# Optimization experiments

Measured on AMD Instinct MI355X. Metric: run time of the kernel, lower is better.

Reference implementation:

```python
import jax, jax.numpy as jnp
import numpy as np

PATCH = 14
NPS = 26  # num_patches_per_side = 364 // 14


def setup_inputs() -> dict:
    key = jax.random.key(0)
    k0, k1, k2 = jax.random.split(key, 3)
    B, C, H, W, D = 32, 3, 364, 364, 1152
    pixel_values = jax.random.normal(k0, (B, C, H, W), dtype=jnp.float32)
    # variable-resolution rectangle masks (top-left aligned, NaViT style)
    rng = np.random.default_rng(0)
    nbh = rng.integers(NPS // 2, NPS + 1, size=B)
    nbw = rng.integers(NPS // 2, NPS + 1, size=B)
    mask = np.zeros((B, NPS, NPS), dtype=bool)
    for i in range(B):  # setup-time only, not part of reference compute
        mask[i, : nbh[i], : nbw[i]] = True
    patch_attention_mask = jnp.asarray(mask)
    conv_w = jax.random.normal(k1, (D, C, PATCH, PATCH), dtype=jnp.float32) * 0.02
    conv_b = jnp.zeros((D,), dtype=jnp.float32)
    pos_emb = jax.random.normal(k2, (NPS * NPS, D), dtype=jnp.float32) * 0.02
    return {
        "pixel_values": pixel_values,
        "patch_attention_mask": patch_attention_mask,
        "conv_w": conv_w,
        "conv_b": conv_b,
        "pos_emb": pos_emb,
    }


def _position_ids(mask):
    # mask: [B, Hp, Wp] bool, True on a top-left rectangle per sample
    B, Hp, Wp = mask.shape
    boundaries = jnp.arange(1, NPS, dtype=jnp.float32) / NPS  # NPS-1 edges
    nb_h = mask[:, :, 0].sum(axis=1)  # [B]
    nb_w = mask[:, 0, :].sum(axis=1)  # [B]
    eps = 1.0 - 1e-6
    frac_h = jnp.arange(Hp, dtype=jnp.float32)[None, :] / nb_h[:, None].astype(jnp.float32) * eps
    frac_w = jnp.arange(Wp, dtype=jnp.float32)[None, :] / nb_w[:, None].astype(jnp.float32) * eps
    # torch.bucketize(right=True) == searchsorted side='right'
    bh = jnp.searchsorted(boundaries, frac_h, side="right")  # [B, Hp]
    bw = jnp.searchsorted(boundaries, frac_w, side="right")  # [B, Wp]
    pos = bh[:, :, None] * NPS + bw[:, None, :]  # [B, Hp, Wp]
    pos = pos.reshape(B, Hp * Wp)
    return jnp.where(mask.reshape(B, -1), pos, 0)


def reference(pixel_values, patch_attention_mask, conv_w, conv_b, pos_emb):
    # patch embedding: conv2d stride=patch, padding VALID
    patch_embeds = jax.lax.conv_general_dilated(
        pixel_values, conv_w,
        window_strides=(PATCH, PATCH), padding="VALID",
        dimension_numbers=("NCHW", "OIHW", "NCHW"),
    ) + conv_b[None, :, None, None]  # [B, D, Hp, Wp]
    B, D, Hp, Wp = patch_embeds.shape
    embeddings = patch_embeds.reshape(B, D, Hp * Wp).transpose(0, 2, 1)  # [B, P, D]
    position_ids = _position_ids(patch_attention_mask)  # [B, P]
    return embeddings + pos_emb[position_ids]
```

## Files before the change

kernel.cpp:

```cpp
#include <hip/hip_runtime.h>
#include <stdint.h>

typedef __attribute__((ext_vector_type(8))) short short8;
typedef __attribute__((ext_vector_type(4))) float f32x4;

#define B_      32
#define C_      3
#define HW_     364
#define D_      1152
#define NPS_    26
#define P_      676
#define K_      588
#define KP_     608
#define KC_     19
#define MT_     64
#define NT_     384
#define AS_     616
#define NP_     21632
#define MBLK_   338
#define NBLK_   3
#define NT16_   72

static __device__ __forceinline__ unsigned short f2bf(float x) {
  unsigned u = __float_as_uint(x);
  u += 0x7fffu + ((u >> 16) & 1u);
  return (unsigned short)(u >> 16);
}

__global__ void prep_weights(const float* __restrict__ w,
                             unsigned short* __restrict__ whi) {
  int idx = blockIdx.x * 256 + threadIdx.x;
  if (idx >= NT16_ * KC_ * 64 * 8) return;
  int e    = idx & 7;
  int lane = (idx >> 3) & 63;
  int t    = idx >> 9;
  int kc   = t % KC_;
  int nt   = t / KC_;
  int n = nt * 16 + (lane & 15);
  int k = kc * 32 + (lane >> 4) * 8 + e;
  float x = (k < K_) ? w[n * K_ + k] : 0.0f;
  whi[idx] = f2bf(x);
}

__global__ void prep_pos(const void* __restrict__ maskp, int* __restrict__ pos_ids) {
  const int word0 = ((const int*)maskp)[0];
  int mode;
  if (word0 == 1) mode = 0;
  else if (word0 == 0x3F800000) mode = 2;
  else mode = 1;

  int idx = blockIdx.x * 256 + threadIdx.x;
  if (idx >= NP_) return;
  const int b = idx / P_;
  const int p = idx - b * P_;
  const int base = b * P_;

  auto get = [&](int i) -> int {
    if (mode == 0) return ((const int*)maskp)[base + i];
    if (mode == 1) return (int)((const unsigned char*)maskp)[base + i];
    return ((const float*)maskp)[base + i] != 0.0f ? 1 : 0;
  };

  int outp = 0;
  if (get(p)) {
    int nbh = 0, nbw = 0;
    #pragma unroll
    for (int r = 0; r < NPS_; ++r) nbh += get(r * NPS_);
    #pragma unroll
    for (int c = 0; c < NPS_; ++c) nbw += get(c);
    const int pr = p / NPS_;
    const int pc = p - pr * NPS_;
    const float eps = 1.0f - 1e-6f;
    const float fh = (float)((double)pr / (double)nbh) * eps;
    const float fw = (float)((double)pc / (double)nbw) * eps;
    int bh = 0, bw = 0;
    #pragma unroll
    for (int k = 1; k < NPS_; ++k) {
      const float bnd = (float)((double)k / (double)NPS_);
      bh += (bnd <= fh) ? 1 : 0;
      bw += (bnd <= fw) ? 1 : 0;
    }
    outp = bh * NPS_ + bw;
  }
  pos_ids[idx] = outp;
}

struct Frags { short8 ah[4]; short8 bh[3]; };

__device__ __forceinline__ void load_frags(Frags& f, int kc, int l15, int lk8,
                                           int ntbase, int lane,
                                           const unsigned short* Ahi_,
                                           const unsigned short* __restrict__ whi) {
  const int ko = kc * 32 + lk8;
  #pragma unroll
  for (int mi = 0; mi < 4; ++mi)
    f.ah[mi] = *(const short8*)&Ahi_[(mi * 16 + l15) * AS_ + ko];
  #pragma unroll
  for (int ni = 0; ni < 3; ++ni) {
    const int off = (((ntbase + ni) * KC_ + kc) * 64 + lane) * 8;
    f.bh[ni] = *(const short8*)(whi + off);
  }
}

__device__ __forceinline__ void mfma_frags(f32x4 acc[4][3], const Frags& f) {
  #pragma unroll
  for (int mi = 0; mi < 4; ++mi)
    #pragma unroll
    for (int ni = 0; ni < 3; ++ni)
      acc[mi][ni] = __builtin_amdgcn_mfma_f32_16x16x32_bf16(f.ah[mi], f.bh[ni], acc[mi][ni], 0, 0, 0);
}

__global__ __launch_bounds__(512, 4)
void fused_embed(const float* __restrict__ pix,
                 const unsigned short* __restrict__ whi,
                 const float* __restrict__ bias,
                 const float* __restrict__ pos_emb,
                 const int* __restrict__ pos_ids,
                 float* __restrict__ out) {
  __shared__ __align__(16) unsigned short Ahi[MT_ * AS_];

  const int bid = blockIdx.x;
  const int mb  = bid / NBLK_;
  const int nb  = bid - mb * NBLK_;
  const int P0  = mb * MT_;
  const int tid = threadIdx.x;

  for (int task = tid; task < 42 * 64; task += 512) {
    const int s  = task >> 6;
    const int p  = task & 63;
    const int c  = s / 14;
    const int rr = s - c * 14;
    const int patch = P0 + p;
    const int b  = patch / P_;
    const int pp = patch - b * P_;
    const int pr = pp / NPS_;
    const int pc = pp - pr * NPS_;
    const float* src = pix + ((size_t)(b * C_ + c) * HW_ + pr * 14 + rr) * HW_ + pc * 14;
    const int kb = c * 196 + rr * 14;
    unsigned short* dh = &Ahi[p * AS_ + kb];
    #pragma unroll
    for (int j = 0; j < 14; j += 2) {
      float x0 = src[j], x1 = src[j + 1];
      *(unsigned*)(dh + j) = (unsigned)f2bf(x0) | ((unsigned)f2bf(x1) << 16);
    }
  }
  for (int i = tid; i < MT_ * 14; i += 512) {
    const int p = i / 14;
    const int k = K_ + (i - p * 14) * 2;
    *(unsigned*)(&Ahi[p * AS_ + k]) = 0u;
  }
  __syncthreads();

  const int lane = tid & 63;
  const int wid  = tid >> 6;
  const int l15  = lane & 15;
  const int lk8  = (lane >> 4) << 3;
  const int ntbase = nb * 24 + wid * 3;

  f32x4 acc[4][3];
  #pragma unroll
  for (int mi = 0; mi < 4; ++mi)
    #pragma unroll
    for (int ni = 0; ni < 3; ++ni)
      acc[mi][ni] = (f32x4)0.0f;

  Frags f0, f1;
  load_frags(f0, 0, l15, lk8, ntbase, lane, Ahi, whi);
  #pragma unroll 1
  for (int kc = 0; kc + 2 < KC_; kc += 2) {
    load_frags(f1, kc + 1, l15, lk8, ntbase, lane, Ahi, whi);
    mfma_frags(acc, f0);
    load_frags(f0, kc + 2, l15, lk8, ntbase, lane, Ahi, whi);
    mfma_frags(acc, f1);
  }
  mfma_frags(acc, f0);

  const int colb = nb * NT_ + wid * 48;
  float cb[3];
  #pragma unroll
  for (int ni = 0; ni < 3; ++ni) cb[ni] = bias[colb + ni * 16 + l15];
  const int r4 = (lane >> 4) * 4;
  #pragma unroll
  for (int mi = 0; mi < 4; ++mi) {
    #pragma unroll
    for (int r = 0; r < 4; ++r) {
      const int patch = P0 + mi * 16 + r4 + r;
      const int pid = pos_ids[patch];
      const float* pe = pos_emb + (size_t)pid * D_;
      float* po = out + (size_t)patch * D_;
      #pragma unroll
      for (int ni = 0; ni < 3; ++ni) {
        const int col = colb + ni * 16 + l15;
        po[col] = acc[mi][ni][r] + cb[ni] + pe[col];
      }
    }
  }
}

extern "C" void kernel_launch(void* const* d_in, const int* in_sizes, int n_in,
                              void* d_out, int out_size, void* d_ws, size_t ws_size,
                              hipStream_t stream) {
  const float* pix            = (const float*)d_in[0];
  const void* mask            = (const void*)d_in[1];
  const float* conv_w         = (const float*)d_in[2];
  const float* conv_b         = (const float*)d_in[3];
  const float* pos_emb        = (const float*)d_in[4];
  float* out                  = (float*)d_out;

  char* ws = (char*)d_ws;
  unsigned short* whi = (unsigned short*)ws;
  int* pos_ids        = (int*)(ws + 1400832);

  prep_weights<<<(NT16_ * KC_ * 64 * 8 + 255) / 256, 256, 0, stream>>>(conv_w, whi);
  prep_pos<<<(NP_ + 255) / 256, 256, 0, stream>>>(mask, pos_ids);
  fused_embed<<<MBLK_ * NBLK_, 512, 0, stream>>>(pix, whi, conv_b, pos_emb, pos_ids, out);
}
```

Measured before the change: 186.5 us.

## Shrink patch tile to 32 and loop over all N blocks per workgroup

Each workgroup now takes 32 patches instead of 64 and walks all three 384-column N blocks in a loop, so the im2col pixel tile is loaded and converted once rather than three times. The grid drops from 1014 to 676 blocks, launch bounds ask for 8 waves per SIMD, and the software double-buffered fragment prefetch is replaced by a simple unprefetched K loop. This cuts redundant pixel reads and bf16 conversion. In exchange, weight loads per output rise because each weight fragment now feeds only 2 M-tiles instead of 4, and the MFMA chain loses its prefetch overlap.

Result: slower. 214.9 us (+15.2%).

```diff
diff --git a/kernel.cpp b/kernel.cpp
--- a/kernel.cpp
+++ b/kernel.cpp
@@ -13,12 +13,11 @@
 #define K_      588
 #define KP_     608
 #define KC_     19
-#define MT_     64
+#define MT_     32
 #define NT_     384
 #define AS_     616
 #define NP_     21632
-#define MBLK_   338
-#define NBLK_   3
+#define GRID_   676
 #define NT16_   72
 
 static __device__ __forceinline__ unsigned short f2bf(float x) {
@@ -85,32 +84,7 @@
   pos_ids[idx] = outp;
 }
 
-struct Frags { short8 ah[4]; short8 bh[3]; };
-
-__device__ __forceinline__ void load_frags(Frags& f, int kc, int l15, int lk8,
-                                           int ntbase, int lane,
-                                           const unsigned short* Ahi_,
-                                           const unsigned short* __restrict__ whi) {
-  const int ko = kc * 32 + lk8;
-  #pragma unroll
-  for (int mi = 0; mi < 4; ++mi)
-    f.ah[mi] = *(const short8*)&Ahi_[(mi * 16 + l15) * AS_ + ko];
-  #pragma unroll
-  for (int ni = 0; ni < 3; ++ni) {
-    const int off = (((ntbase + ni) * KC_ + kc) * 64 + lane) * 8;
-    f.bh[ni] = *(const short8*)(whi + off);
-  }
-}
-
-__device__ __forceinline__ void mfma_frags(f32x4 acc[4][3], const Frags& f) {
-  #pragma unroll
-  for (int mi = 0; mi < 4; ++mi)
-    #pragma unroll
-    for (int ni = 0; ni < 3; ++ni)
-      acc[mi][ni] = __builtin_amdgcn_mfma_f32_16x16x32_bf16(f.ah[mi], f.bh[ni], acc[mi][ni], 0, 0, 0);
-}
-
-__global__ __launch_bounds__(512, 4)
+__global__ __launch_bounds__(512, 8)
 void fused_embed(const float* __restrict__ pix,
                  const unsigned short* __restrict__ whi,
                  const float* __restrict__ bias,
@@ -119,15 +93,13 @@
                  float* __restrict__ out) {
   __shared__ __align__(16) unsigned short Ahi[MT_ * AS_];
 
-  const int bid = blockIdx.x;
-  const int mb  = bid / NBLK_;
-  const int nb  = bid - mb * NBLK_;
+  const int mb  = blockIdx.x;
   const int P0  = mb * MT_;
   const int tid = threadIdx.x;
 
-  for (int task = tid; task < 42 * 64; task += 512) {
-    const int s  = task >> 6;
-    const int p  = task & 63;
+  for (int task = tid; task < 42 * MT_; task += 512) {
+    const int s  = task >> 5;
+    const int p  = task & 31;
     const int c  = s / 14;
     const int rr = s - c * 14;
     const int patch = P0 + p;
@@ -135,14 +107,11 @@
     const int pp = patch - b * P_;
     const int pr = pp / NPS_;
     const int pc = pp - pr * NPS_;
-    const float* src = pix + ((size_t)(b * C_ + c) * HW_ + pr * 14 + rr) * HW_ + pc * 14;
-    const int kb = c * 196 + rr * 14;
-    unsigned short* dh = &Ahi[p * AS_ + kb];
+    const float* sr = pix + ((size_t)(b * C_ + c) * HW_ + pr * 14 + rr) * HW_ + pc * 14;
+    unsigned* dh = (unsigned*)&Ahi[p * AS_ + c * 196 + rr * 14];
     #pragma unroll
-    for (int j = 0; j < 14; j += 2) {
-      float x0 = src[j], x1 = src[j + 1];
-      *(unsigned*)(dh + j) = (unsigned)f2bf(x0) | ((unsigned)f2bf(x1) << 16);
-    }
+    for (int j = 0; j < 7; ++j)
+      dh[j] = (unsigned)f2bf(sr[2 * j]) | ((unsigned)f2bf(sr[2 * j + 1]) << 16);
   }
   for (int i = tid; i < MT_ * 14; i += 512) {
     const int p = i / 14;
@@ -155,43 +124,50 @@
   const int wid  = tid >> 6;
   const int l15  = lane & 15;
   const int lk8  = (lane >> 4) << 3;
-  const int ntbase = nb * 24 + wid * 3;
+  const int r4   = (lane >> 4) * 4;
 
-  f32x4 acc[4][3];
-  #pragma unroll
-  for (int mi = 0; mi < 4; ++mi)
+  #pragma unroll 1
+  for (int nb = 0; nb < 3; ++nb) {
+    const int ntbase = nb * 24 + wid * 3;
+
+    f32x4 acc[2][3];
     #pragma unroll
-    for (int ni = 0; ni < 3; ++ni)
-      acc[mi][ni] = (f32x4)0.0f;
+    for (int mi = 0; mi < 2; ++mi)
+      #pragma unroll
+      for (int ni = 0; ni < 3; ++ni)
+        acc[mi][ni] = (f32x4)0.0f;
 
-  Frags f0, f1;
-  load_frags(f0, 0, l15, lk8, ntbase, lane, Ahi, whi);
-  #pragma unroll 1
-  for (int kc = 0; kc + 2 < KC_; kc += 2) {
-    load_frags(f1, kc + 1, l15, lk8, ntbase, lane, Ahi, whi);
-    mfma_frags(acc, f0);
-    load_frags(f0, kc + 2, l15, lk8, ntbase, lane, Ahi, whi);
-    mfma_frags(acc, f1);
-  }
-  mfma_frags(acc, f0);
+    #pragma unroll 1
+    for (int kc = 0; kc < KC_; ++kc) {
+      const int ko = kc * 32 + lk8;
+      short8 ah0 = *(const short8*)&Ahi[l15 * AS_ + ko];
+      short8 ah1 = *(const short8*)&Ahi[(16 + l15) * AS_ + ko];
+      short8 bh0 = *(const short8*)(whi + (((ntbase + 0) * KC_ + kc) * 64 + lane) * 8);
+      short8 bh1 = *(const short8*)(whi + (((ntbase + 1) * KC_ + kc) * 64 + lane) * 8);
+      short8 bh2 = *(const short8*)(whi + (((ntbase + 2) * KC_ + kc) * 64 + lane) * 8);
+      acc[0][0] = __builtin_amdgcn_mfma_f32_16x16x32_bf16(ah0, bh0, acc[0][0], 0, 0, 0);
+      acc[0][1] = __builtin_amdgcn_mfma_f32_16x16x32_bf16(ah0, bh1, acc[0][1], 0, 0, 0);
+      acc[0][2] = __builtin_amdgcn_mfma_f32_16x16x32_bf16(ah0, bh2, acc[0][2], 0, 0, 0);
+      acc[1][0] = __builtin_amdgcn_mfma_f32_16x16x32_bf16(ah1, bh0, acc[1][0], 0, 0, 0);
+      acc[1][1] = __builtin_amdgcn_mfma_f32_16x16x32_bf16(ah1, bh1, acc[1][1], 0, 0, 0);
+      acc[1][2] = __builtin_amdgcn_mfma_f32_16x16x32_bf16(ah1, bh2, acc[1][2], 0, 0, 0);
+    }
 
-  const int colb = nb * NT_ + wid * 48;
-  float cb[3];
-  #pragma unroll
-  for (int ni = 0; ni < 3; ++ni) cb[ni] = bias[colb + ni * 16 + l15];
-  const int r4 = (lane >> 4) * 4;
-  #pragma unroll
-  for (int mi = 0; mi < 4; ++mi) {
+    const int colb = nb * NT_ + wid * 48;
+    float cb0 = bias[colb + l15];
+    float cb1 = bias[colb + 16 + l15];
+    float cb2 = bias[colb + 32 + l15];
     #pragma unroll
-    for (int r = 0; r < 4; ++r) {
-      const int patch = P0 + mi * 16 + r4 + r;
-      const int pid = pos_ids[patch];
-      const float* pe = pos_emb + (size_t)pid * D_;
-      float* po = out + (size_t)patch * D_;
+    for (int mi = 0; mi < 2; ++mi) {
       #pragma unroll
-      for (int ni = 0; ni < 3; ++ni) {
-        const int col = colb + ni * 16 + l15;
-        po[col] = acc[mi][ni][r] + cb[ni] + pe[col];
+      for (int r = 0; r < 4; ++r) {
+        const int patch = P0 + mi * 16 + r4 + r;
+        const int pid = pos_ids[patch];
+        const float* pe = pos_emb + (size_t)pid * D_;
+        float* po = out + (size_t)patch * D_;
+        po[colb + l15]      = acc[mi][0][r] + cb0 + pe[colb + l15];
+        po[colb + 16 + l15] = acc[mi][1][r] + cb1 + pe[colb + 16 + l15];
+        po[colb + 32 + l15] = acc[mi][2][r] + cb2 + pe[colb + 32 + l15];
       }
     }
   }
@@ -213,5 +189,5 @@
 
   prep_weights<<<(NT16_ * KC_ * 64 * 8 + 255) / 256, 256, 0, stream>>>(conv_w, whi);
   prep_pos<<<(NP_ + 255) / 256, 256, 0, stream>>>(mask, pos_ids);
-  fused_embed<<<MBLK_ * NBLK_, 512, 0, stream>>>(pix, whi, conv_b, pos_emb, pos_ids, out);
+  fused_embed<<<GRID_, 512, 0, stream>>>(pix, whi, conv_b, pos_emb, pos_ids, out);
 }
```
